# Kernel optimization log

Hardware: AMD Instinct MI355X
Metric: run time of the kernel (lower is better)

## Reference

```python
import jax, jax.numpy as jnp
import numpy as np
import math

B, S, HID, H = 2, 4096, 512, 8
D_K = HID // H


def setup_inputs() -> dict:
    key = jax.random.key(0)
    ks = jax.random.split(key, 8)
    inp = {
        "query": jax.random.normal(ks[0], (B, S, HID), dtype=jnp.float32),
        "key": jax.random.normal(ks[1], (B, S, HID), dtype=jnp.float32),
        "value": jax.random.normal(ks[2], (B, S, HID), dtype=jnp.float32),
        "mask": jax.random.randint(ks[3], (B, S), 0, 2, dtype=jnp.int32),
        # conv1d kernel_size=1, bias=False -> plain [out,in] weights (xavier-normal-ish)
        "Wq": jax.random.normal(ks[4], (HID, HID), dtype=jnp.float32) * (1.0 / math.sqrt(HID)),
        "Wk": jax.random.normal(ks[5], (HID, HID), dtype=jnp.float32) * (1.0 / math.sqrt(HID)),
        "Wv": jax.random.normal(ks[6], (HID, HID), dtype=jnp.float32) * (1.0 / math.sqrt(HID)),
        "Wo": jax.random.normal(ks[7], (HID, HID), dtype=jnp.float32) * (1.0 / math.sqrt(HID)),
    }
    return inp


def reference(query, key, value, mask, Wq, Wk, Wv, Wo):
    b, s, _ = query.shape
    # conv1d(k=1, bias=False) projection == x @ W.T; split heads -> [b,h,s,d_k]
    def proj(x, W):
        return jnp.einsum('bsd,ed->bse', x, W).reshape(b, s, H, D_K).transpose(0, 2, 1, 3)
    q, k, v = proj(query, Wq), proj(key, Wk), proj(value, Wv)
    # NOTE: original scales by 1/log(d_k), not 1/sqrt(d_k)
    score = jnp.einsum('bhqd,bhkd->bhqk', q, k) / math.log(D_K)
    m = mask.reshape(b, 1, 1, s)  # broadcast over heads and query positions
    score = jnp.where(m == 0, jnp.float32(-1e30), score)
    attn = jax.nn.softmax(score, axis=-1)  # dropout is identity in eval
    x = jnp.einsum('bhqk,bhkd->bhqd', attn, v)
    x = x.transpose(0, 2, 1, 3).reshape(b, s, HID)
    return jnp.einsum('bsd,ed->bse', x, Wo)
```

## Files before the change

### kernel.cpp

```cpp
#include <hip/hip_runtime.h>
#include <hip/hip_bf16.h>
#include <cstdint>
#include <cstddef>


namespace {

constexpr int kB = 2, kS = 4096, kHid = 512, kH = 8, kDk = 64;
constexpr int kBH = kB * kH;
constexpr int kM = kB * kS;

typedef __attribute__((ext_vector_type(8))) short short8;
typedef __attribute__((ext_vector_type(4))) float floatx4;
typedef unsigned short u16;

__device__ __forceinline__ u16 bf16rne(float f) {
    uint32_t u = __float_as_uint(f);
    u += 0x7fffu + ((u >> 16) & 1u);
    return (u16)(u >> 16);
}
__device__ __forceinline__ uint32_t pk2(float lo, float hi) {
#if __has_builtin(__builtin_amdgcn_cvt_pk_bf16_f32)
    typedef __attribute__((ext_vector_type(2))) __bf16 bf2;
    bf2 h = __builtin_amdgcn_cvt_pk_bf16_f32(lo, hi);
    return __builtin_bit_cast(uint32_t, h);
#else
    return ((uint32_t)bf16rne(hi) << 16) | (uint32_t)bf16rne(lo);
#endif
}
__device__ __forceinline__ float fexp2(float x) {
#if __has_builtin(__builtin_amdgcn_exp2f)
    return __builtin_amdgcn_exp2f(x);
#else
    return exp2f(x);
#endif
}

__global__ __launch_bounds__(256) void cvt_qw(const float* __restrict__ q,
    const float* __restrict__ k, const float* __restrict__ v,
    const float* __restrict__ w0, const float* __restrict__ w1,
    const float* __restrict__ w2, const float* __restrict__ w3,
    u16* __restrict__ xall, u16* __restrict__ wall) {
    const int bx = blockIdx.x;
    if (bx < 12288) {
        int z = bx >> 12;
        size_t i = (size_t)(bx & 4095) * 256 + threadIdx.x;
        const float* src = z == 0 ? q : (z == 1 ? k : v);
        float4 f = ((const float4*)src)[i];
        ushort4 o;
        o.x = bf16rne(f.x); o.y = bf16rne(f.y);
        o.z = bf16rne(f.z); o.w = bf16rne(f.w);
        ((ushort4*)(xall + (size_t)z * kM * kHid))[i] = o;
    } else {
        int r = bx - 12288;
        int z = r >> 8;
        size_t i = (size_t)(r & 255) * 256 + threadIdx.x;
        const float* src = z == 0 ? w0 : (z == 1 ? w1 : (z == 2 ? w2 : w3));
        float sc = (z == 0)
            ? (float)(1.4426950408889634 / (6.0 * 0.6931471805599453))
            : 1.0f;
        float4 f = ((const float4*)src)[i];
        ushort4 o;
        o.x = bf16rne(f.x * sc); o.y = bf16rne(f.y * sc);
        o.z = bf16rne(f.z * sc); o.w = bf16rne(f.w * sc);
        ((ushort4*)(wall + (size_t)z * kHid * kHid))[i] = o;
    }
}

__global__ __launch_bounds__(256) void cvt_mask(const int* __restrict__ mask,
    float* __restrict__ fb) {
    int i = blockIdx.x * 256 + threadIdx.x;
    fb[i] = mask[i] ? 0.0f : -1e30f;
}

__global__ __launch_bounds__(256, 3) void proj(const u16* __restrict__ xall,
    const u16* __restrict__ wall, u16* __restrict__ qp, u16* __restrict__ kp,
    u16* __restrict__ vt) {
    __shared__ float smt[4][16][68];
    const int z = blockIdx.z;
    const u16* x = xall + (size_t)z * kM * kHid;
    const u16* w = wall + (size_t)z * kHid * kHid;
    const int wv = threadIdx.x >> 6, lane = threadIdx.x & 63;
    const int quad = lane >> 4, l16 = lane & 15;
    const int mb = blockIdx.y * 128 + (wv >> 1) * 64;
    const int nb = blockIdx.x * 128 + (wv & 1) * 64;
    floatx4 acc[4][4] = {};
    const u16* xr = x + (size_t)(mb + l16) * kHid + quad * 8;
    const u16* wr = w + (size_t)(nb + l16) * kHid + quad * 8;
    for (int k0 = 0; k0 < kHid; k0 += 32) {
        short8 a[4], bt[4];
#pragma unroll
        for (int i = 0; i < 4; i++)
            a[i] = *(const short8*)(xr + (size_t)i * 16 * kHid + k0);
#pragma unroll
        for (int t = 0; t < 4; t++)
            bt[t] = *(const short8*)(wr + (size_t)t * 16 * kHid + k0);
#pragma unroll
        for (int i = 0; i < 4; i++)
#pragma unroll
        for (int t = 0; t < 4; t++)
            acc[i][t] = __builtin_amdgcn_mfma_f32_16x16x32_bf16(a[i], bt[t], acc[i][t], 0, 0, 0);
    }
    if (z < 2) {
        u16* dst = (z == 0) ? qp : kp;
        const int row16 = lane >> 2, cseg = (lane & 3) * 16;
#pragma unroll
        for (int i = 0; i < 4; i++) {
#pragma unroll
            for (int t = 0; t < 4; t++)
#pragma unroll
            for (int r = 0; r < 4; r++)
                smt[wv][quad * 4 + r][t * 16 + l16] = acc[i][t][r];
            __builtin_amdgcn_wave_barrier();
            const float* rp = &smt[wv][row16][cseg];
            float4 f0 = *(const float4*)(rp);
            float4 f1 = *(const float4*)(rp + 4);
            float4 f2 = *(const float4*)(rp + 8);
            float4 f3 = *(const float4*)(rp + 12);
            uint4 o0, o1;
            o0.x = pk2(f0.x, f0.y); o0.y = pk2(f0.z, f0.w);
            o0.z = pk2(f1.x, f1.y); o0.w = pk2(f1.z, f1.w);
            o1.x = pk2(f2.x, f2.y); o1.y = pk2(f2.z, f2.w);
            o1.z = pk2(f3.x, f3.y); o1.w = pk2(f3.z, f3.w);
            u16* dp = dst + (size_t)(mb + i * 16 + row16) * kHid + nb + cseg;
            *(uint4*)dp = o0;
            *(uint4*)(dp + 8) = o1;
            __builtin_amdgcn_wave_barrier();
        }
    } else {
#pragma unroll
        for (int i = 0; i < 4; i++)
#pragma unroll
        for (int t = 0; t < 4; t++) {
            int m0 = mb + i * 16 + quad * 4;
            int n = nb + t * 16 + l16;
            int b = m0 >> 12, s = m0 & (kS - 1);
            int h = n >> 6,   d = n & (kDk - 1);
            ushort4 o;
            o.x = bf16rne(acc[i][t][0]); o.y = bf16rne(acc[i][t][1]);
            o.z = bf16rne(acc[i][t][2]); o.w = bf16rne(acc[i][t][3]);
            *(ushort4*)(vt + ((size_t)(b * kH + h) * kDk + d) * kS + s) = o;
        }
    }
}

__global__ __launch_bounds__(256, 2) void attn(const u16* __restrict__ qp,
    const u16* __restrict__ kp, const u16* __restrict__ vt,
    const float* __restrict__ fbias, u16* __restrict__ xo) {
    union SmT {
        struct { u16 K[2][64][64]; u16 V[2][64][64]; u16 P[4][32][72]; } s;
        float ep[4][32][68];
    };
    __shared__ __align__(16) SmT sm;
    const int tid = threadIdx.x;
    const int wv = tid >> 6, lane = tid & 63;
    const int quad = lane >> 4, l16 = lane & 15;
    const int bh = blockIdx.y, b = bh >> 3, h = bh & 7;
    const int q0 = blockIdx.x * 128 + wv * 32;
    const u16* Qb = qp + (size_t)b * kS * kHid + h * 64;
    const u16* Kb = kp + (size_t)b * kS * kHid + h * 64;
    const u16* Vb = vt + (size_t)bh * kDk * kS;
    const float* fm = fbias + b * kS;

    short8 qf[2][2];
#pragma unroll
    for (int qt = 0; qt < 2; qt++)
#pragma unroll
    for (int hh = 0; hh < 2; hh++)
        qf[qt][hh] = *(const short8*)(Qb + (size_t)(q0 + qt * 16 + l16) * kHid + hh * 32 + quad * 8);

    floatx4 O[2][4] = {};
    float rs[2] = {0.0f, 0.0f};

    const int srow = tid >> 3;
    const int sc   = (tid & 7) * 8;
    const int pc   = ((tid & 7) ^ (srow & 7)) * 8;
    const int cA = (quad ^ (l16 & 7)) * 8;

    short8 rk[2], rv[2];
    rk[0] = *(const short8*)(Kb + (size_t)srow * kHid + sc);
    rk[1] = *(const short8*)(Kb + (size_t)(srow + 32) * kHid + sc);
    rv[0] = *(const short8*)(Vb + (size_t)srow * kS + sc);
    rv[1] = *(const short8*)(Vb + (size_t)(srow + 32) * kS + sc);
    *(short8*)&sm.s.K[0][srow][pc]      = rk[0];
    *(short8*)&sm.s.K[0][srow + 32][pc] = rk[1];
    *(short8*)&sm.s.V[0][srow][pc]      = rv[0];
    *(short8*)&sm.s.V[0][srow + 32][pc] = rv[1];
    rk[0] = *(const short8*)(Kb + (size_t)(64 + srow) * kHid + sc);
    rk[1] = *(const short8*)(Kb + (size_t)(64 + srow + 32) * kHid + sc);
    rv[0] = *(const short8*)(Vb + (size_t)srow * kS + 64 + sc);
    rv[1] = *(const short8*)(Vb + (size_t)(srow + 32) * kS + 64 + sc);
    __syncthreads();

    for (int it = 0; it < 64; ++it) {
        const int p = it & 1;
        const int kt = it * 64;
        *(short8*)&sm.s.K[1 - p][srow][pc]      = rk[0];
        *(short8*)&sm.s.K[1 - p][srow + 32][pc] = rk[1];
        *(short8*)&sm.s.V[1 - p][srow][pc]      = rv[0];
        *(short8*)&sm.s.V[1 - p][srow + 32][pc] = rv[1];
        {
            const int kt2 = ((it + 2) & 63) * 64;
            rk[0] = *(const short8*)(Kb + (size_t)(kt2 + srow) * kHid + sc);
            rk[1] = *(const short8*)(Kb + (size_t)(kt2 + srow + 32) * kHid + sc);
            rv[0] = *(const short8*)(Vb + (size_t)srow * kS + kt2 + sc);
            rv[1] = *(const short8*)(Vb + (size_t)(srow + 32) * kS + kt2 + sc);
        }
        float4 fb[4];
#pragma unroll
        for (int t = 0; t < 4; t++)
            fb[t] = *(const float4*)(fm + kt + t * 16 + quad * 4);
        short8 kf[4][2], vf[4][2];
#pragma unroll
        for (int t = 0; t < 4; t++) {
            kf[t][0] = *(const short8*)&sm.s.K[p][t * 16 + l16][cA];
            kf[t][1] = *(const short8*)&sm.s.K[p][t * 16 + l16][cA ^ 32];
            vf[t][0] = *(const short8*)&sm.s.V[p][t * 16 + l16][cA];
            vf[t][1] = *(const short8*)&sm.s.V[p][t * 16 + l16][cA ^ 32];
        }
#pragma unroll
        for (int qt = 0; qt < 2; qt++) {
            floatx4 st[4];
#pragma unroll
            for (int t = 0; t < 4; t++) {
                floatx4 z = {fb[t].x, fb[t].y, fb[t].z, fb[t].w};
                z = __builtin_amdgcn_mfma_f32_16x16x32_bf16(kf[t][0], qf[qt][0], z, 0, 0, 0);
                st[t] = __builtin_amdgcn_mfma_f32_16x16x32_bf16(kf[t][1], qf[qt][1], z, 0, 0, 0);
            }
            u16* prow = &sm.s.P[wv][qt * 16 + l16][0];
            float sum = 0.0f;
#pragma unroll
            for (int t = 0; t < 4; t++) {
                float p0 = fexp2(st[t][0]);
                float p1 = fexp2(st[t][1]);
                float p2 = fexp2(st[t][2]);
                float p3 = fexp2(st[t][3]);
                sum += (p0 + p1) + (p2 + p3);
                uint2 w2; w2.x = pk2(p0, p1); w2.y = pk2(p2, p3);
                *(uint2*)(prow + t * 16 + quad * 4) = w2;
            }
            rs[qt] += sum;
        }
        __builtin_amdgcn_wave_barrier();
#pragma unroll
        for (int qt = 0; qt < 2; qt++) {
            short8 ap0 = *(const short8*)&sm.s.P[wv][qt * 16 + l16][quad * 8];
            short8 ap1 = *(const short8*)&sm.s.P[wv][qt * 16 + l16][32 + quad * 8];
#pragma unroll
            for (int td = 0; td < 4; td++) {
                O[qt][td] = __builtin_amdgcn_mfma_f32_16x16x32_bf16(vf[td][0], ap0, O[qt][td], 0, 0, 0);
                O[qt][td] = __builtin_amdgcn_mfma_f32_16x16x32_bf16(vf[td][1], ap1, O[qt][td], 0, 0, 0);
            }
        }
        __syncthreads();
    }

    float inv[2];
#pragma unroll
    for (int qt = 0; qt < 2; qt++) {
        float r = rs[qt];
        r += __shfl_xor(r, 16);
        r += __shfl_xor(r, 32);
        inv[qt] = 1.0f / r;
    }
#pragma unroll
    for (int qt = 0; qt < 2; qt++)
#pragma unroll
    for (int td = 0; td < 4; td++) {
        floatx4 o4 = O[qt][td];
        o4[0] *= inv[qt]; o4[1] *= inv[qt]; o4[2] *= inv[qt]; o4[3] *= inv[qt];
        *(floatx4*)&sm.ep[wv][qt * 16 + l16][td * 16 + quad * 4] = o4;
    }
    __builtin_amdgcn_wave_barrier();
    {
        const int qloc = lane >> 1, half = lane & 1;
        const float* row = &sm.ep[wv][qloc][half * 32];
        u16* orow = xo + ((size_t)(b * kS + q0 + qloc)) * kHid + h * 64 + half * 32;
#pragma unroll
        for (int j = 0; j < 4; j++) {
            float4 f0 = *(const float4*)(row + j * 8);
            float4 f1 = *(const float4*)(row + j * 8 + 4);
            uint4 o;
            o.x = pk2(f0.x, f0.y); o.y = pk2(f0.z, f0.w);
            o.z = pk2(f1.x, f1.y); o.w = pk2(f1.z, f1.w);
            *(uint4*)(orow + j * 8) = o;
        }
    }
}

__global__ __launch_bounds__(256, 3) void oproj(const u16* __restrict__ x,
    const u16* __restrict__ w, float* __restrict__ out) {
    const int wv = threadIdx.x >> 6, lane = threadIdx.x & 63;
    const int quad = lane >> 4, l16 = lane & 15;
    const int mb = blockIdx.y * 128 + (wv >> 1) * 64;
    const int nb = blockIdx.x * 128 + (wv & 1) * 64;
    floatx4 acc[4][4] = {};
    const u16* xr = x + (size_t)(mb + l16) * kHid + quad * 8;
    const u16* wr = w + (size_t)(nb + l16) * kHid + quad * 8;
    for (int k0 = 0; k0 < kHid; k0 += 32) {
        short8 a[4], bt[4];
#pragma unroll
        for (int i = 0; i < 4; i++)
            a[i] = *(const short8*)(xr + (size_t)i * 16 * kHid + k0);
#pragma unroll
        for (int t = 0; t < 4; t++)
            bt[t] = *(const short8*)(wr + (size_t)t * 16 * kHid + k0);
#pragma unroll
        for (int i = 0; i < 4; i++)
#pragma unroll
        for (int t = 0; t < 4; t++)
            acc[i][t] = __builtin_amdgcn_mfma_f32_16x16x32_bf16(a[i], bt[t], acc[i][t], 0, 0, 0);
    }
#pragma unroll
    for (int i = 0; i < 4; i++)
#pragma unroll
    for (int t = 0; t < 4; t++)
#pragma unroll
    for (int r = 0; r < 4; r++) {
        int m = mb + i * 16 + quad * 4 + r;
        int n = nb + t * 16 + l16;
        out[(size_t)m * kHid + n] = acc[i][t][r];
    }
}

}

extern "C" void kernel_launch(void* const* d_in, const int* in_sizes, int n_in,
                              void* d_out, int out_size, void* d_ws, size_t ws_size,
                              hipStream_t stream) {
    const float* q  = (const float*)d_in[0];
    const float* k  = (const float*)d_in[1];
    const float* v  = (const float*)d_in[2];
    const int* mask = (const int*)d_in[3];
    const float* w0 = (const float*)d_in[4];
    const float* w1 = (const float*)d_in[5];
    const float* w2 = (const float*)d_in[6];
    const float* w3 = (const float*)d_in[7];
    float* out = (float*)d_out;

    u16* ws   = (u16*)d_ws;
    u16* xall = ws;
    u16* wall = xall + (size_t)3 * kM * kHid;
    u16* qp   = wall + (size_t)4 * kHid * kHid;
    u16* kp   = qp + (size_t)kBH * kS * kDk;
    u16* vt   = kp + (size_t)kBH * kS * kDk;
    u16* xo   = xall;
    float* fbias = (float*)(xall + (size_t)kM * kHid);

    dim3 blk(256);
    cvt_qw <<<dim3(13312), blk, 0, stream>>>(q, k, v, w0, w1, w2, w3, xall, wall);
    proj   <<<dim3(kHid / 128, kM / 128, 3), blk, 0, stream>>>(xall, wall, qp, kp, vt);
    cvt_mask<<<dim3(kB * kS / 256), blk, 0, stream>>>(mask, fbias);
    attn   <<<dim3(kS / 128, kBH), blk, 0, stream>>>(qp, kp, vt, fbias, xo);
    oproj  <<<dim3(kHid / 128, kM / 128), blk, 0, stream>>>(
        xo, wall + (size_t)3 * kHid * kHid, out);
}
```

Baseline: 269.8 us.

## Use 512-thread attention blocks with 16 query rows per wave

The attention kernel now runs 8 waves per block instead of 4. Each wave handles 16 query rows instead of 32, while the block still covers 128 queries. Each thread now loads one K and one V vector per tile, and per-wave registers (O accumulators, Q fragments) are halved, aiming for higher occupancy and better latency hiding. The cost is that every wave still reads the full K/V fragments from LDS for half the MFMA work, and each __syncthreads now has to coordinate twice as many waves.

```diff
diff --git a/kernel.cpp b/kernel.cpp
--- a/kernel.cpp
+++ b/kernel.cpp
@@ -144,72 +144,55 @@
     }
 }
 
-__global__ __launch_bounds__(256, 2) void attn(const u16* __restrict__ qp,
+__global__ __launch_bounds__(512, 4) void attn(const u16* __restrict__ qp,
     const u16* __restrict__ kp, const u16* __restrict__ vt,
     const float* __restrict__ fbias, u16* __restrict__ xo) {
     union SmT {
-        struct { u16 K[2][64][64]; u16 V[2][64][64]; u16 P[4][32][72]; } s;
-        float ep[4][32][68];
+        struct { u16 K[2][64][64]; u16 V[2][64][64]; u16 P[8][16][72]; } s;
+        float ep[8][16][68];
     };
     __shared__ __align__(16) SmT sm;
     const int tid = threadIdx.x;
     const int wv = tid >> 6, lane = tid & 63;
     const int quad = lane >> 4, l16 = lane & 15;
     const int bh = blockIdx.y, b = bh >> 3, h = bh & 7;
-    const int q0 = blockIdx.x * 128 + wv * 32;
+    const int q0 = blockIdx.x * 128 + wv * 16;
     const u16* Qb = qp + (size_t)b * kS * kHid + h * 64;
     const u16* Kb = kp + (size_t)b * kS * kHid + h * 64;
     const u16* Vb = vt + (size_t)bh * kDk * kS;
     const float* fm = fbias + b * kS;
 
-    short8 qf[2][2];
-#pragma unroll
-    for (int qt = 0; qt < 2; qt++)
-#pragma unroll
-    for (int hh = 0; hh < 2; hh++)
-        qf[qt][hh] = *(const short8*)(Qb + (size_t)(q0 + qt * 16 + l16) * kHid + hh * 32 + quad * 8);
-
-    floatx4 O[2][4] = {};
-    float rs[2] = {0.0f, 0.0f};
+    short8 qf[2];
+    qf[0] = *(const short8*)(Qb + (size_t)(q0 + l16) * kHid + quad * 8);
+    qf[1] = *(const short8*)(Qb + (size_t)(q0 + l16) * kHid + 32 + quad * 8);
+
+    floatx4 O[4] = {};
+    float rs = 0.0f;
 
     const int srow = tid >> 3;
     const int sc   = (tid & 7) * 8;
     const int pc   = ((tid & 7) ^ (srow & 7)) * 8;
     const int cA = (quad ^ (l16 & 7)) * 8;
 
-    short8 rk[2], rv[2];
-    rk[0] = *(const short8*)(Kb + (size_t)srow * kHid + sc);
-    rk[1] = *(const short8*)(Kb + (size_t)(srow + 32) * kHid + sc);
-    rv[0] = *(const short8*)(Vb + (size_t)srow * kS + sc);
-    rv[1] = *(const short8*)(Vb + (size_t)(srow + 32) * kS + sc);
-    *(short8*)&sm.s.K[0][srow][pc]      = rk[0];
-    *(short8*)&sm.s.K[0][srow + 32][pc] = rk[1];
-    *(short8*)&sm.s.V[0][srow][pc]      = rv[0];
-    *(short8*)&sm.s.V[0][srow + 32][pc] = rv[1];
-    rk[0] = *(const short8*)(Kb + (size_t)(64 + srow) * kHid + sc);
-    rk[1] = *(const short8*)(Kb + (size_t)(64 + srow + 32) * kHid + sc);
-    rv[0] = *(const short8*)(Vb + (size_t)srow * kS + 64 + sc);
-    rv[1] = *(const short8*)(Vb + (size_t)(srow + 32) * kS + 64 + sc);
+    short8 rk, rv;
+    rk = *(const short8*)(Kb + (size_t)srow * kHid + sc);
+    rv = *(const short8*)(Vb + (size_t)srow * kS + sc);
+    *(short8*)&sm.s.K[0][srow][pc] = rk;
+    *(short8*)&sm.s.V[0][srow][pc] = rv;
+    rk = *(const short8*)(Kb + (size_t)(64 + srow) * kHid + sc);
+    rv = *(const short8*)(Vb + (size_t)srow * kS + 64 + sc);
     __syncthreads();
 
     for (int it = 0; it < 64; ++it) {
         const int p = it & 1;
         const int kt = it * 64;
-        *(short8*)&sm.s.K[1 - p][srow][pc]      = rk[0];
-        *(short8*)&sm.s.K[1 - p][srow + 32][pc] = rk[1];
-        *(short8*)&sm.s.V[1 - p][srow][pc]      = rv[0];
-        *(short8*)&sm.s.V[1 - p][srow + 32][pc] = rv[1];
+        *(short8*)&sm.s.K[1 - p][srow][pc] = rk;
+        *(short8*)&sm.s.V[1 - p][srow][pc] = rv;
         {
             const int kt2 = ((it + 2) & 63) * 64;
-            rk[0] = *(const short8*)(Kb + (size_t)(kt2 + srow) * kHid + sc);
-            rk[1] = *(const short8*)(Kb + (size_t)(kt2 + srow + 32) * kHid + sc);
-            rv[0] = *(const short8*)(Vb + (size_t)srow * kS + kt2 + sc);
-            rv[1] = *(const short8*)(Vb + (size_t)(srow + 32) * kS + kt2 + sc);
-        }
-        float4 fb[4];
-#pragma unroll
-        for (int t = 0; t < 4; t++)
-            fb[t] = *(const float4*)(fm + kt + t * 16 + quad * 4);
+            rk = *(const short8*)(Kb + (size_t)(kt2 + srow) * kHid + sc);
+            rv = *(const short8*)(Vb + (size_t)srow * kS + kt2 + sc);
+        }
         short8 kf[4][2], vf[4][2];
 #pragma unroll
         for (int t = 0; t < 4; t++) {
@@ -218,16 +201,15 @@
             vf[t][0] = *(const short8*)&sm.s.V[p][t * 16 + l16][cA];
             vf[t][1] = *(const short8*)&sm.s.V[p][t * 16 + l16][cA ^ 32];
         }
-#pragma unroll
-        for (int qt = 0; qt < 2; qt++) {
-            floatx4 st[4];
-#pragma unroll
-            for (int t = 0; t < 4; t++) {
-                floatx4 z = {fb[t].x, fb[t].y, fb[t].z, fb[t].w};
-                z = __builtin_amdgcn_mfma_f32_16x16x32_bf16(kf[t][0], qf[qt][0], z, 0, 0, 0);
-                st[t] = __builtin_amdgcn_mfma_f32_16x16x32_bf16(kf[t][1], qf[qt][1], z, 0, 0, 0);
-            }
-            u16* prow = &sm.s.P[wv][qt * 16 + l16][0];
+        floatx4 st[4];
+#pragma unroll
+        for (int t = 0; t < 4; t++) {
+            floatx4 z = *(const floatx4*)(fm + kt + t * 16 + quad * 4);
+            z = __builtin_amdgcn_mfma_f32_16x16x32_bf16(kf[t][0], qf[0], z, 0, 0, 0);
+            st[t] = __builtin_amdgcn_mfma_f32_16x16x32_bf16(kf[t][1], qf[1], z, 0, 0, 0);
+        }
+        {
+            u16* prow = &sm.s.P[wv][l16][0];
             float sum = 0.0f;
 #pragma unroll
             for (int t = 0; t < 4; t++) {
@@ -239,45 +221,41 @@
                 uint2 w2; w2.x = pk2(p0, p1); w2.y = pk2(p2, p3);
                 *(uint2*)(prow + t * 16 + quad * 4) = w2;
             }
-            rs[qt] += sum;
+            rs += sum;
         }
         __builtin_amdgcn_wave_barrier();
-#pragma unroll
-        for (int qt = 0; qt < 2; qt++) {
-            short8 ap0 = *(const short8*)&sm.s.P[wv][qt * 16 + l16][quad * 8];
-            short8 ap1 = *(const short8*)&sm.s.P[wv][qt * 16 + l16][32 + quad * 8];
+        {
+            short8 ap0 = *(const short8*)&sm.s.P[wv][l16][quad * 8];
+            short8 ap1 = *(const short8*)&sm.s.P[wv][l16][32 + quad * 8];
 #pragma unroll
             for (int td = 0; td < 4; td++) {
-                O[qt][td] = __builtin_amdgcn_mfma_f32_16x16x32_bf16(vf[td][0], ap0, O[qt][td], 0, 0, 0);
-                O[qt][td] = __builtin_amdgcn_mfma_f32_16x16x32_bf16(vf[td][1], ap1, O[qt][td], 0, 0, 0);
+                O[td] = __builtin_amdgcn_mfma_f32_16x16x32_bf16(vf[td][0], ap0, O[td], 0, 0, 0);
+                O[td] = __builtin_amdgcn_mfma_f32_16x16x32_bf16(vf[td][1], ap1, O[td], 0, 0, 0);
             }
         }
         __syncthreads();
     }
 
-    float inv[2];
-#pragma unroll
-    for (int qt = 0; qt < 2; qt++) {
-        float r = rs[qt];
+    float inv;
+    {
+        float r = rs;
         r += __shfl_xor(r, 16);
         r += __shfl_xor(r, 32);
-        inv[qt] = 1.0f / r;
-    }
-#pragma unroll
-    for (int qt = 0; qt < 2; qt++)
+        inv = 1.0f / r;
+    }
 #pragma unroll
     for (int td = 0; td < 4; td++) {
-        floatx4 o4 = O[qt][td];
-        o4[0] *= inv[qt]; o4[1] *= inv[qt]; o4[2] *= inv[qt]; o4[3] *= inv[qt];
-        *(floatx4*)&sm.ep[wv][qt * 16 + l16][td * 16 + quad * 4] = o4;
+        floatx4 o4 = O[td];
+        o4[0] *= inv; o4[1] *= inv; o4[2] *= inv; o4[3] *= inv;
+        *(floatx4*)&sm.ep[wv][l16][td * 16 + quad * 4] = o4;
     }
     __builtin_amdgcn_wave_barrier();
     {
-        const int qloc = lane >> 1, half = lane & 1;
-        const float* row = &sm.ep[wv][qloc][half * 32];
-        u16* orow = xo + ((size_t)(b * kS + q0 + qloc)) * kHid + h * 64 + half * 32;
-#pragma unroll
-        for (int j = 0; j < 4; j++) {
+        const int qloc = lane >> 2, seg = (lane & 3) * 16;
+        const float* row = &sm.ep[wv][qloc][seg];
+        u16* orow = xo + ((size_t)(b * kS + q0 + qloc)) * kHid + h * 64 + seg;
+#pragma unroll
+        for (int j = 0; j < 2; j++) {
             float4 f0 = *(const float4*)(row + j * 8);
             float4 f1 = *(const float4*)(row + j * 8 + 4);
             uint4 o;
@@ -351,7 +329,7 @@
     cvt_qw <<<dim3(13312), blk, 0, stream>>>(q, k, v, w0, w1, w2, w3, xall, wall);
     proj   <<<dim3(kHid / 128, kM / 128, 3), blk, 0, stream>>>(xall, wall, qp, kp, vt);
     cvt_mask<<<dim3(kB * kS / 256), blk, 0, stream>>>(mask, fbias);
-    attn   <<<dim3(kS / 128, kBH), blk, 0, stream>>>(qp, kp, vt, fbias, xo);
+    attn   <<<dim3(kS / 128, kBH), dim3(512), 0, stream>>>(qp, kp, vt, fbias, xo);
     oproj  <<<dim3(kHid / 128, kM / 128), blk, 0, stream>>>(
         xo, wall + (size_t)3 * kHid * kHid, out);
 }
```

Result: no change. 268.1 us (-0.6%).
